# Kernel optimization log

Measured on AMD Instinct MI355X. Metric: run time of the kernel, lower is better.

The kernel has to match this reference:

```python
import jax, jax.numpy as jnp
import numpy as np

B, S, ENC_D, DEC_D, ATTN_D, OUT_D = 32, 2048, 1024, 1024, 1024, 1024
SCALING = 1.0


def setup_inputs() -> dict:
    key = jax.random.key(0)
    ks = jax.random.split(key, 10)
    enc_states = jax.random.normal(ks[0], (B, S, ENC_D), dtype=jnp.float32)
    # lengths in [S//2, S] so every row has at least one valid position
    enc_len = jax.random.randint(ks[1], (B,), S // 2, S + 1, dtype=jnp.int32)
    dec_states = jax.random.normal(ks[2], (B, DEC_D), dtype=jnp.float32)
    s = 0.02
    W_enc = jax.random.normal(ks[3], (ENC_D, ATTN_D), dtype=jnp.float32) * s
    b_enc = jnp.zeros((ATTN_D,), dtype=jnp.float32)
    W_dec = jax.random.normal(ks[4], (DEC_D, ATTN_D), dtype=jnp.float32) * s
    b_dec = jnp.zeros((ATTN_D,), dtype=jnp.float32)
    w_attn = jax.random.normal(ks[5], (ATTN_D,), dtype=jnp.float32) * s
    W_out = jax.random.normal(ks[6], (ENC_D, OUT_D), dtype=jnp.float32) * s
    b_out = jnp.zeros((OUT_D,), dtype=jnp.float32)
    return {
        "enc_states": enc_states,
        "dec_states": dec_states,
        "W_enc": W_enc, "b_enc": b_enc,
        "W_dec": W_dec, "b_dec": b_dec,
        "w_attn": w_attn,
        "W_out": W_out, "b_out": b_out,
        "enc_len": enc_len,
    }


def reference(enc_states, dec_states, W_enc, b_enc, W_dec, b_dec, w_attn, W_out, b_out, enc_len):
    # precomputed_enc_h = mlp_enc(enc_states): [B, S, ATTN_D]
    enc_h = jnp.einsum("bse,ea->bsa", enc_states, W_enc) + b_enc
    # dec_h = mlp_dec(dec_states): [B, ATTN_D]
    dec_h = dec_states @ W_dec + b_dec
    # additive (Bahdanau) score: tanh(enc_h + dec_h) . w_attn -> [B, S]
    attn = jnp.einsum("bsa,a->bs", jnp.tanh(enc_h + dec_h[:, None, :]), w_attn)
    # length mask
    mask = jnp.arange(enc_states.shape[1])[None, :] < enc_len[:, None]  # [B, S]
    attn = jnp.where(mask, attn, -jnp.inf)
    attn = jax.nn.softmax(attn * SCALING, axis=-1)
    # context = attn @ enc_states -> [B, ENC_D]
    context = jnp.einsum("bs,bse->be", attn, enc_states)
    context = context @ W_out + b_out
    return (context, attn)
```

## Files before the change

kernel.cpp:

```cpp
#include <hip/hip_runtime.h>
#include <cstdint>
#include <cstddef>

#define BATCH 32
#define SEQ   2048
#define DIM   1024
#define MROWS (BATCH*SEQ)

typedef __attribute__((ext_vector_type(4))) float  floatx4;
typedef __attribute__((ext_vector_type(8))) short  short8;

__device__ __forceinline__ unsigned short f2bf(float f) {
  unsigned int u = __float_as_uint(f);
  u += 0x7fffu + ((u >> 16) & 1u);
  return (unsigned short)(u >> 16);
}

__device__ __forceinline__ void async16(const void* g, void* l) {
  __builtin_amdgcn_global_load_lds(
      (const __attribute__((address_space(1))) unsigned int*)g,
      (__attribute__((address_space(3))) unsigned int*)l, 16, 0, 0);
}

__device__ __forceinline__ float fast_tanh(float x) {
  float e = __expf(2.0f * x);
  return 1.0f - 2.0f * __builtin_amdgcn_rcpf(1.0f + e);
}

__global__ void k_prep(const float* __restrict__ W_enc, unsigned short* __restrict__ Wt,
                       const float* __restrict__ dec, const float* __restrict__ W_dec,
                       const float* __restrict__ b_dec, const float* __restrict__ b_enc,
                       float* __restrict__ dech) {
  __shared__ float tile[32][33];
  int blk = blockIdx.x;
  int tid = threadIdx.x;
  if (blk < 1024) {
    int n0 = (blk & 31) * 32, k0 = (blk >> 5) * 32;
    int tx = tid & 31, ty = tid >> 5;
#pragma unroll
    for (int i = 0; i < 4; ++i) {
      int y = ty + i * 8;
      tile[y][tx] = W_enc[(size_t)(k0 + y) * DIM + n0 + tx];
    }
    __syncthreads();
#pragma unroll
    for (int i = 0; i < 4; ++i) {
      int y = ty + i * 8;
      Wt[(size_t)(n0 + y) * DIM + k0 + tx] = f2bf(tile[tx][y]);
    }
  } else {
    int db = blk - 1024;
    int ax = db & 3, bgi = (db >> 2) & 3, z = db >> 4;
    int a  = ax * 256 + tid;
    int bg = bgi * 8;
    float bias = (z == 0) ? (b_dec[a] + b_enc[a]) : 0.0f;
    float acc[8];
#pragma unroll
    for (int j = 0; j < 8; ++j) acc[j] = bias;
    const float* wcp = W_dec + (size_t)z * 128 * DIM + a;
#pragma unroll 4
    for (int e = 0; e < 128; ++e) {
      float w = wcp[(size_t)e * DIM];
#pragma unroll
      for (int j = 0; j < 8; ++j)
        acc[j] = fmaf(dec[(size_t)(bg + j) * DIM + z * 128 + e], w, acc[j]);
    }
#pragma unroll
    for (int j = 0; j < 8; ++j)
      atomicAdd(&dech[(size_t)(bg + j) * DIM + a], acc[j]);
  }
}

#define PH_BAR do { asm volatile("" ::: "memory"); __builtin_amdgcn_s_barrier(); asm volatile("" ::: "memory"); } while(0)
#define SCHED0 __builtin_amdgcn_sched_barrier(0)
#define SP1 __builtin_amdgcn_s_setprio(1)
#define SP0 __builtin_amdgcn_s_setprio(0)
#define VMCNT(n) asm volatile("s_waitcnt vmcnt(" #n ")" ::: "memory")
#define LGKM0 asm volatile("s_waitcnt lgkmcnt(0)" ::: "memory")

__global__ void __launch_bounds__(512, 2) k_gemm256(
    const float* __restrict__ enc,
    const unsigned short* __restrict__ Wt,
    const float* __restrict__ dech,
    const float* __restrict__ w_attn,
    const int* __restrict__ enc_len,
    float* __restrict__ score)
{
  int bid = blockIdx.x;
  int t  = (bid & 7) * 128 + (bid >> 3);
  int nb = t & 3;
  int rt = t >> 2;
  int bb = rt >> 3;
  int len = enc_len[bb];
  if (((rt & 7) * 256) >= len) return;

  __shared__ __align__(16) char lds[131072];

  int tid = threadIdx.x;
  int w = tid >> 6, lane = tid & 63;
  int wr = w >> 2;
  int wc = w & 3;
  int li = lane & 15, g = lane >> 4;
  int xl = (li & 7) << 4;

  const char* Agc = (const char*)enc + (size_t)rt * 256 * 4096;
  const char* Bg  = (const char*)(Wt + (size_t)nb * 256 * DIM);

  size_t sbase = (size_t)((lane >> 3) * 2048 +
                 (((lane & 7) << 4) ^ (((lane >> 3) & 7) << 4)));
  size_t swoff = (size_t)(w * 2) * 16384;
  int    ldbase = w * 2048;

#define STAGE_B(buf, h, kt) do { \
  async16(Bg + sbase + swoff + (size_t)(h) * 262144 + (size_t)(kt) * 128, \
          lds + 65536 + (buf) * 32768 + ldbase + (h) * 16384); \
  async16(Bg + sbase + swoff + 16384 + (size_t)(h) * 262144 + (size_t)(kt) * 128, \
          lds + 65536 + (buf) * 32768 + ldbase + 1024 + (h) * 16384); \
} while (0)

  size_t aoff = (size_t)(w * 16 + (lane >> 3)) * 4096 +
                (size_t)(((lane & 7) ^ (lane >> 3)) * 32);
  float4 aR[2][2][2];

#define LOAD_A(kt) do { \
  _Pragma("unroll") for (int c = 0; c < 2; ++c) { \
    const char* g0_ = Agc + aoff + (size_t)(c * 8) * 4096 + (size_t)(kt) * 256; \
    aR[0][c][0] = *(const float4*)(g0_); \
    aR[0][c][1] = *(const float4*)(g0_ + 16); \
  } \
} while (0)
#define LOAD_A1(kt) do { \
  _Pragma("unroll") for (int c = 0; c < 2; ++c) { \
    const char* g1_ = Agc + aoff + (size_t)(128 + c * 8) * 4096 + (size_t)(kt) * 256; \
    aR[1][c][0] = *(const float4*)(g1_); \
    aR[1][c][1] = *(const float4*)(g1_ + 16); \
  } \
} while (0)
#define WRITE_A(buf) do { \
  _Pragma("unroll") for (int h_ = 0; h_ < 2; ++h_) \
  _Pragma("unroll") for (int c_ = 0; c_ < 2; ++c_) { \
    float4 u0_ = aR[h_][c_][0], u1_ = aR[h_][c_][1]; \
    short8 pk_; \
    pk_[0] = (short)f2bf(u0_.x); pk_[1] = (short)f2bf(u0_.y); \
    pk_[2] = (short)f2bf(u0_.z); pk_[3] = (short)f2bf(u0_.w); \
    pk_[4] = (short)f2bf(u1_.x); pk_[5] = (short)f2bf(u1_.y); \
    pk_[6] = (short)f2bf(u1_.z); pk_[7] = (short)f2bf(u1_.w); \
    *(short8*)(lds + (buf) * 32768 + h_ * 16384 + w * 2048 + c_ * 1024 + lane * 16) = pk_; \
  } \
} while (0)

  short8 sA0[2][2], sA1[2][2];
  short8 aX[2][2];
  short8 bX[2][2];
  floatx4 acc[8][4] = {};

#define RD_A2(buf, f0, DST) do { \
  const char* base_ = lds + (buf) * 32768 + (wr * 128 + (f0) * 16 + li) * 128; \
  int c0_ = (g * 16) ^ xl; \
  _Pragma("unroll") for (int j = 0; j < 2; ++j) { \
    DST[j][0] = *(const short8*)(base_ + j * 2048 + c0_); \
    DST[j][1] = *(const short8*)(base_ + j * 2048 + (c0_ ^ 64)); \
  } \
} while (0)
#define RD_B(buf, nh, DST) do { \
  const char* base_ = lds + 65536 + (buf) * 32768 + (wc * 64 + (nh) * 32 + li) * 128; \
  int c0_ = (g * 16) ^ xl; \
  _Pragma("unroll") for (int tnq = 0; tnq < 2; ++tnq) { \
    DST[tnq][0] = *(const short8*)(base_ + tnq * 2048 + c0_); \
    DST[tnq][1] = *(const short8*)(base_ + tnq * 2048 + (c0_ ^ 64)); \
  } \
} while (0)
#define MFMA_Q(mh, nh, ALO, AHI, BB) do { \
  _Pragma("unroll") for (int ks = 0; ks < 2; ++ks) \
  _Pragma("unroll") for (int tnq = 0; tnq < 2; ++tnq) { \
    acc[(mh)*4+0][(nh)*2+tnq] = __builtin_amdgcn_mfma_f32_16x16x32_bf16(ALO[0][ks], BB[tnq][ks], acc[(mh)*4+0][(nh)*2+tnq], 0, 0, 0); \
    acc[(mh)*4+1][(nh)*2+tnq] = __builtin_amdgcn_mfma_f32_16x16x32_bf16(ALO[1][ks], BB[tnq][ks], acc[(mh)*4+1][(nh)*2+tnq], 0, 0, 0); \
    acc[(mh)*4+2][(nh)*2+tnq] = __builtin_amdgcn_mfma_f32_16x16x32_bf16(AHI[0][ks], BB[tnq][ks], acc[(mh)*4+2][(nh)*2+tnq], 0, 0, 0); \
    acc[(mh)*4+3][(nh)*2+tnq] = __builtin_amdgcn_mfma_f32_16x16x32_bf16(AHI[1][ks], BB[tnq][ks], acc[(mh)*4+3][(nh)*2+tnq], 0, 0, 0); \
  } \
} while (0)

#define TILE_STEP(CUR, KT2, MODE, SP_, SQ_) do { \
   \
  RD_A2(CUR, 2, aX); \
  RD_B(CUR, 0, bX); \
  if ((MODE) == 0) { LOAD_A(KT2); } \
  PH_BAR; SCHED0; SP1; MFMA_Q(0, 0, SP_, aX, bX); SP0; SCHED0; \
  PH_BAR; \
   \
  RD_B(CUR, 1, SQ_); \
  if ((MODE) == 0) { LOAD_A1(KT2); } \
  PH_BAR; SCHED0; SP1; MFMA_Q(0, 1, SP_, aX, SQ_); SP0; SCHED0; \
  PH_BAR; \
   \
  if ((MODE) == 0) { STAGE_B(CUR, 0, KT2); STAGE_B(CUR, 1, KT2); } \
  RD_A2(CUR, 4, SP_); \
  RD_A2(CUR, 6, aX); \
  PH_BAR; SCHED0; SP1; MFMA_Q(1, 1, SP_, aX, SQ_); SP0; SCHED0; \
  PH_BAR; \
   \
  if ((MODE) == 0) { VMCNT(4); WRITE_A(CUR); } \
  else if ((MODE) == 1) { VMCNT(0); } \
  if ((MODE) < 2) RD_A2((CUR) ^ 1, 0, SQ_); \
  PH_BAR; SCHED0; SP1; MFMA_Q(1, 0, SP_, aX, bX); SP0; SCHED0; \
  PH_BAR; \
} while (0)

  LOAD_A(0); LOAD_A1(0);
  VMCNT(0);
  WRITE_A(0);
  LOAD_A(1); LOAD_A1(1);
  STAGE_B(0, 0, 0); STAGE_B(0, 1, 0);
  STAGE_B(1, 0, 1); STAGE_B(1, 1, 1);
  VMCNT(4);
  WRITE_A(1);
  LGKM0;
  PH_BAR;
  RD_A2(0, 0, sA0);

#pragma unroll 1
  for (int u = 0; u < 14; u += 2) {
    TILE_STEP(0, u + 2, 0, sA0, sA1);
    TILE_STEP(1, u + 3, 0, sA1, sA0);
  }
  TILE_STEP(0, 0, 1, sA0, sA1);
  TILE_STEP(1, 0, 2, sA1, sA0);

  float dh[4], wa[4];
#pragma unroll
  for (int tn = 0; tn < 4; ++tn) {
    int n = nb * 256 + wc * 64 + tn * 16 + li;
    dh[tn] = dech[(size_t)bb * DIM + n];
    wa[tn] = w_attn[n];
  }
#pragma unroll
  for (int tm = 0; tm < 8; ++tm) {
    int mrow = rt * 256 + wr * 128 + tm * 16 + g * 4;
#pragma unroll
    for (int r = 0; r < 4; ++r) {
      float v = 0.0f;
#pragma unroll
      for (int tn = 0; tn < 4; ++tn)
        v = fmaf(wa[tn], fast_tanh(acc[tm][tn][r] + dh[tn]), v);
      v += __shfl_xor(v, 1);
      v += __shfl_xor(v, 2);
      v += __shfl_xor(v, 4);
      v += __shfl_xor(v, 8);
      if (li == 0) atomicAdd(&score[mrow + r], v);
    }
  }
#undef TILE_STEP
#undef MFMA_Q
#undef RD_B
#undef RD_A2
#undef WRITE_A
#undef LOAD_A1
#undef LOAD_A
#undef STAGE_B
}

__global__ void k_softmax(const float* __restrict__ score, const int* __restrict__ enc_len,
                          float* __restrict__ attn) {
  int b = blockIdx.x, tid = threadIdx.x;
  int len = enc_len[b];
  __shared__ float red[256];
  float v[8];
  float m = -1e30f;
#pragma unroll
  for (int i = 0; i < 8; ++i) {
    int s = tid + i * 256;
    v[i] = score[(size_t)b * SEQ + s];
    if (s < len) m = fmaxf(m, v[i]);
  }
  red[tid] = m; __syncthreads();
  for (int st = 128; st > 0; st >>= 1) {
    if (tid < st) red[tid] = fmaxf(red[tid], red[tid + st]);
    __syncthreads();
  }
  float mx = red[0]; __syncthreads();
  float sum = 0.0f;
#pragma unroll
  for (int i = 0; i < 8; ++i) {
    int s = tid + i * 256;
    float e = (s < len) ? __expf(v[i] - mx) : 0.0f;
    v[i] = e; sum += e;
  }
  red[tid] = sum; __syncthreads();
  for (int st = 128; st > 0; st >>= 1) {
    if (tid < st) red[tid] += red[tid + st];
    __syncthreads();
  }
  float inv = 1.0f / red[0];
#pragma unroll
  for (int i = 0; i < 8; ++i)
    attn[(size_t)b * SEQ + tid + i * 256] = v[i] * inv;
}

__global__ void k_context(const float* __restrict__ enc, const float* __restrict__ attn,
                          const int* __restrict__ enc_len, float* __restrict__ ctx) {
  int b = blockIdx.y, sc = blockIdx.x;
  int len = enc_len[b];
  int s0 = sc * 32;
  if (s0 >= len) return;
  int cnt = min(32, len - s0);
  int tid = threadIdx.x;
  const float* base = enc + ((size_t)b * SEQ + s0) * DIM + tid * 4;
  const float* ap   = attn + (size_t)b * SEQ + s0;
  float a0 = 0.f, a1 = 0.f, a2 = 0.f, a3 = 0.f;
  int i = 0;
  for (; i + 8 <= cnt; i += 8) {
    float4 x[8];
    float  w[8];
#pragma unroll
    for (int u = 0; u < 8; ++u)
      x[u] = *(const float4*)(base + (size_t)(i + u) * DIM);
#pragma unroll
    for (int u = 0; u < 8; ++u)
      w[u] = ap[i + u];
#pragma unroll
    for (int u = 0; u < 8; ++u) {
      a0 = fmaf(w[u], x[u].x, a0); a1 = fmaf(w[u], x[u].y, a1);
      a2 = fmaf(w[u], x[u].z, a2); a3 = fmaf(w[u], x[u].w, a3);
    }
  }
  for (; i < cnt; ++i) {
    float w = ap[i];
    float4 x = *(const float4*)(base + (size_t)i * DIM);
    a0 = fmaf(w, x.x, a0); a1 = fmaf(w, x.y, a1);
    a2 = fmaf(w, x.z, a2); a3 = fmaf(w, x.w, a3);
  }
  float* c = ctx + (size_t)b * DIM + tid * 4;
  atomicAdd(c + 0, a0); atomicAdd(c + 1, a1);
  atomicAdd(c + 2, a2); atomicAdd(c + 3, a3);
}

__global__ void k_out(const float* __restrict__ ctx, const float* __restrict__ W_out,
                      const float* __restrict__ b_out, float* __restrict__ out) {
  int o  = blockIdx.x * 256 + threadIdx.x;
  int bg = blockIdx.y * 8;
  int z  = blockIdx.z;
  float bias = (z == 0) ? b_out[o] : 0.0f;
  float acc[8];
#pragma unroll
  for (int j = 0; j < 8; ++j) acc[j] = bias;
  const float* wc = W_out + (size_t)z * 128 * DIM + o;
#pragma unroll 4
  for (int e = 0; e < 128; ++e) {
    float w = wc[(size_t)e * DIM];
#pragma unroll
    for (int j = 0; j < 8; ++j)
      acc[j] = fmaf(ctx[(size_t)(bg + j) * DIM + z * 128 + e], w, acc[j]);
  }
#pragma unroll
  for (int j = 0; j < 8; ++j)
    atomicAdd(&out[(size_t)(bg + j) * DIM + o], acc[j]);
}

extern "C" void kernel_launch(void* const* d_in, const int* in_sizes, int n_in,
                              void* d_out, int out_size, void* d_ws, size_t ws_size,
                              hipStream_t stream) {
  (void)in_sizes; (void)n_in; (void)out_size; (void)ws_size;
  const float* enc_states = (const float*)d_in[0];
  const float* dec_states = (const float*)d_in[1];
  const float* W_enc      = (const float*)d_in[2];
  const float* b_enc      = (const float*)d_in[3];
  const float* W_dec      = (const float*)d_in[4];
  const float* b_dec      = (const float*)d_in[5];
  const float* w_attn     = (const float*)d_in[6];
  const float* W_out      = (const float*)d_in[7];
  const float* b_out      = (const float*)d_in[8];
  const int*   enc_len    = (const int*)  d_in[9];

  float* out_ctx  = (float*)d_out;
  float* out_attn = (float*)d_out + BATCH * DIM;

  char* ws = (char*)d_ws;
  unsigned short* Wt  = (unsigned short*)ws;
  float* score = (float*)(ws + (2u << 20));
  float* ctx   = (float*)(ws + (2u << 20) + 262144);
  float* dech  = (float*)(ws + (2u << 20) + 262144 + 131072);

  hipMemsetAsync(ws + (2u << 20), 0, 262144 + 131072 + 131072, stream);
  hipMemsetAsync(d_out, 0, (size_t)BATCH * DIM * sizeof(float), stream);

  k_prep<<<1152, 256, 0, stream>>>(W_enc, Wt, dec_states, W_dec, b_dec, b_enc, dech);
  k_gemm256<<<1024, 512, 0, stream>>>(enc_states, Wt, dech, w_attn, enc_len, score);
  k_softmax<<<BATCH, 256, 0, stream>>>(score, enc_len, out_attn);
  k_context<<<dim3(64, BATCH), 256, 0, stream>>>(enc_states, out_attn, enc_len, ctx);
  k_out<<<dim3(4, 4, 8), 256, 0, stream>>>(ctx, W_out, b_out, out_ctx);
}
```

Measured before the change: 671.8 us.

## Pre-convert encoder states to bf16 and make each GEMM block sweep all N tiles

Encoder states are now converted to bf16 once in the prep kernel, for valid rows only, and written to a workspace buffer. The GEMM loads A tiles asynchronously into LDS instead of converting them per block. The GEMM grid shrinks from 1024 to 256 blocks, and each block loops over all four 256-column N tiles with an epilogue after each. This removes the fourfold re-reading and re-conversion of fp32 activations, at the cost of an extra write and read pass over a bf16 copy. Only 256 blocks at 2 per CU may underfill the GPU, and the masked-out tail blocks now leave whole CUs idle.

```diff
diff --git a/kernel.cpp b/kernel.cpp
--- a/kernel.cpp
+++ b/kernel.cpp
@@ -27,7 +27,9 @@
   return 1.0f - 2.0f * __builtin_amdgcn_rcpf(1.0f + e);
 }
 
-__global__ void k_prep(const float* __restrict__ W_enc, unsigned short* __restrict__ Wt,
+__global__ void k_prep(const float* __restrict__ enc, const int* __restrict__ enc_len,
+                       unsigned short* __restrict__ Abf,
+                       const float* __restrict__ W_enc, unsigned short* __restrict__ Wt,
                        const float* __restrict__ dec, const float* __restrict__ W_dec,
                        const float* __restrict__ b_dec, const float* __restrict__ b_enc,
                        float* __restrict__ dech) {
@@ -48,7 +50,7 @@
       int y = ty + i * 8;
       Wt[(size_t)(n0 + y) * DIM + k0 + tx] = f2bf(tile[tx][y]);
     }
-  } else {
+  } else if (blk < 1152) {
     int db = blk - 1024;
     int ax = db & 3, bgi = (db >> 2) & 3, z = db >> 4;
     int a  = ax * 256 + tid;
@@ -68,6 +70,21 @@
 #pragma unroll
     for (int j = 0; j < 8; ++j)
       atomicAdd(&dech[(size_t)(bg + j) * DIM + a], acc[j]);
+  } else {
+    int cv = blk - 1152;
+    int b = cv >> 8, rc = cv & 255;
+    int r0 = rc * 8;
+    if (r0 >= enc_len[b]) return;
+    size_t base = ((size_t)b * SEQ + r0) * DIM;
+    const float4* src = (const float4*)(enc + base);
+    ushort4* dst = (ushort4*)(Abf + base);
+#pragma unroll
+    for (int i = 0; i < 8; ++i) {
+      float4 v = src[tid + i * 256];
+      ushort4 h;
+      h.x = f2bf(v.x); h.y = f2bf(v.y); h.z = f2bf(v.z); h.w = f2bf(v.w);
+      dst[tid + i * 256] = h;
+    }
   }
 }
 
@@ -76,20 +93,16 @@
 #define SP1 __builtin_amdgcn_s_setprio(1)
 #define SP0 __builtin_amdgcn_s_setprio(0)
 #define VMCNT(n) asm volatile("s_waitcnt vmcnt(" #n ")" ::: "memory")
-#define LGKM0 asm volatile("s_waitcnt lgkmcnt(0)" ::: "memory")
 
 __global__ void __launch_bounds__(512, 2) k_gemm256(
-    const float* __restrict__ enc,
+    const unsigned short* __restrict__ Abf,
     const unsigned short* __restrict__ Wt,
     const float* __restrict__ dech,
     const float* __restrict__ w_attn,
     const int* __restrict__ enc_len,
     float* __restrict__ score)
 {
-  int bid = blockIdx.x;
-  int t  = (bid & 7) * 128 + (bid >> 3);
-  int nb = t & 3;
-  int rt = t >> 2;
+  int rt = blockIdx.x;
   int bb = rt >> 3;
   int len = enc_len[bb];
   if (((rt & 7) * 256) >= len) return;
@@ -103,50 +116,27 @@
   int li = lane & 15, g = lane >> 4;
   int xl = (li & 7) << 4;
 
-  const char* Agc = (const char*)enc + (size_t)rt * 256 * 4096;
-  const char* Bg  = (const char*)(Wt + (size_t)nb * 256 * DIM);
+  const char* Ag = (const char*)(Abf + (size_t)rt * 256 * DIM);
+  const char* Bg = (const char*)Wt;
 
   size_t sbase = (size_t)((lane >> 3) * 2048 +
                  (((lane & 7) << 4) ^ (((lane >> 3) & 7) << 4)));
   size_t swoff = (size_t)(w * 2) * 16384;
   int    ldbase = w * 2048;
 
-#define STAGE_B(buf, h, kt) do { \
-  async16(Bg + sbase + swoff + (size_t)(h) * 262144 + (size_t)(kt) * 128, \
+#define STAGE_A(buf, h, V) do { \
+  size_t ka_ = (size_t)((V) & 15) * 128; \
+  async16(Ag + sbase + swoff + (size_t)(h) * 262144 + ka_, \
+          lds + (buf) * 32768 + ldbase + (h) * 16384); \
+  async16(Ag + sbase + swoff + 16384 + (size_t)(h) * 262144 + ka_, \
+          lds + (buf) * 32768 + ldbase + 1024 + (h) * 16384); \
+} while (0)
+#define STAGE_B(buf, h, V) do { \
+  size_t kb_ = (size_t)((V) >> 4) * 524288 + (size_t)((V) & 15) * 128; \
+  async16(Bg + kb_ + sbase + swoff + (size_t)(h) * 262144, \
           lds + 65536 + (buf) * 32768 + ldbase + (h) * 16384); \
-  async16(Bg + sbase + swoff + 16384 + (size_t)(h) * 262144 + (size_t)(kt) * 128, \
+  async16(Bg + kb_ + sbase + swoff + 16384 + (size_t)(h) * 262144, \
           lds + 65536 + (buf) * 32768 + ldbase + 1024 + (h) * 16384); \
-} while (0)
-
-  size_t aoff = (size_t)(w * 16 + (lane >> 3)) * 4096 +
-                (size_t)(((lane & 7) ^ (lane >> 3)) * 32);
-  float4 aR[2][2][2];
-
-#define LOAD_A(kt) do { \
-  _Pragma("unroll") for (int c = 0; c < 2; ++c) { \
-    const char* g0_ = Agc + aoff + (size_t)(c * 8) * 4096 + (size_t)(kt) * 256; \
-    aR[0][c][0] = *(const float4*)(g0_); \
-    aR[0][c][1] = *(const float4*)(g0_ + 16); \
-  } \
-} while (0)
-#define LOAD_A1(kt) do { \
-  _Pragma("unroll") for (int c = 0; c < 2; ++c) { \
-    const char* g1_ = Agc + aoff + (size_t)(128 + c * 8) * 4096 + (size_t)(kt) * 256; \
-    aR[1][c][0] = *(const float4*)(g1_); \
-    aR[1][c][1] = *(const float4*)(g1_ + 16); \
-  } \
-} while (0)
-#define WRITE_A(buf) do { \
-  _Pragma("unroll") for (int h_ = 0; h_ < 2; ++h_) \
-  _Pragma("unroll") for (int c_ = 0; c_ < 2; ++c_) { \
-    float4 u0_ = aR[h_][c_][0], u1_ = aR[h_][c_][1]; \
-    short8 pk_; \
-    pk_[0] = (short)f2bf(u0_.x); pk_[1] = (short)f2bf(u0_.y); \
-    pk_[2] = (short)f2bf(u0_.z); pk_[3] = (short)f2bf(u0_.w); \
-    pk_[4] = (short)f2bf(u1_.x); pk_[5] = (short)f2bf(u1_.y); \
-    pk_[6] = (short)f2bf(u1_.z); pk_[7] = (short)f2bf(u1_.w); \
-    *(short8*)(lds + (buf) * 32768 + h_ * 16384 + w * 2048 + c_ * 1024 + lane * 16) = pk_; \
-  } \
 } while (0)
 
   short8 sA0[2][2], sA1[2][2];
@@ -180,83 +170,77 @@
   } \
 } while (0)
 
-#define TILE_STEP(CUR, KT2, MODE, SP_, SQ_) do { \
-   \
+#define TILE_STEP(CUR, V2, MODE, SP_, SQ_) do { \
   RD_A2(CUR, 2, aX); \
   RD_B(CUR, 0, bX); \
-  if ((MODE) == 0) { LOAD_A(KT2); } \
   PH_BAR; SCHED0; SP1; MFMA_Q(0, 0, SP_, aX, bX); SP0; SCHED0; \
   PH_BAR; \
-   \
   RD_B(CUR, 1, SQ_); \
-  if ((MODE) == 0) { LOAD_A1(KT2); } \
   PH_BAR; SCHED0; SP1; MFMA_Q(0, 1, SP_, aX, SQ_); SP0; SCHED0; \
   PH_BAR; \
-   \
-  if ((MODE) == 0) { STAGE_B(CUR, 0, KT2); STAGE_B(CUR, 1, KT2); } \
+  if ((MODE) == 0) { STAGE_B(CUR, 0, V2); STAGE_B(CUR, 1, V2); } \
   RD_A2(CUR, 4, SP_); \
   RD_A2(CUR, 6, aX); \
   PH_BAR; SCHED0; SP1; MFMA_Q(1, 1, SP_, aX, SQ_); SP0; SCHED0; \
   PH_BAR; \
-   \
-  if ((MODE) == 0) { VMCNT(4); WRITE_A(CUR); } \
-  else if ((MODE) == 1) { VMCNT(0); } \
+  if ((MODE) == 0) { STAGE_A(CUR, 0, V2); STAGE_A(CUR, 1, V2); } \
+  if ((MODE) == 0) { VMCNT(8); } else if ((MODE) == 1) { VMCNT(0); } \
   if ((MODE) < 2) RD_A2((CUR) ^ 1, 0, SQ_); \
   PH_BAR; SCHED0; SP1; MFMA_Q(1, 0, SP_, aX, bX); SP0; SCHED0; \
   PH_BAR; \
 } while (0)
 
-  LOAD_A(0); LOAD_A1(0);
-  VMCNT(0);
-  WRITE_A(0);
-  LOAD_A(1); LOAD_A1(1);
-  STAGE_B(0, 0, 0); STAGE_B(0, 1, 0);
-  STAGE_B(1, 0, 1); STAGE_B(1, 1, 1);
-  VMCNT(4);
-  WRITE_A(1);
-  LGKM0;
+#define EPI(NB) do { \
+  float dh_[4], wa_[4]; \
+  _Pragma("unroll") for (int tn = 0; tn < 4; ++tn) { \
+    int n_ = (NB) * 256 + wc * 64 + tn * 16 + li; \
+    dh_[tn] = dech[(size_t)bb * DIM + n_]; \
+    wa_[tn] = w_attn[n_]; \
+  } \
+  _Pragma("unroll") for (int tm = 0; tm < 8; ++tm) { \
+    int mrow_ = rt * 256 + wr * 128 + tm * 16 + g * 4; \
+    _Pragma("unroll") for (int r = 0; r < 4; ++r) { \
+      float v_ = 0.0f; \
+      _Pragma("unroll") for (int tn = 0; tn < 4; ++tn) \
+        v_ = fmaf(wa_[tn], fast_tanh(acc[tm][tn][r] + dh_[tn]), v_); \
+      v_ += __shfl_xor(v_, 1); \
+      v_ += __shfl_xor(v_, 2); \
+      v_ += __shfl_xor(v_, 4); \
+      v_ += __shfl_xor(v_, 8); \
+      if (li == 0) atomicAdd(&score[mrow_ + r], v_); \
+    } \
+  } \
+  _Pragma("unroll") for (int tm = 0; tm < 8; ++tm) \
+  _Pragma("unroll") for (int tn = 0; tn < 4; ++tn) \
+  _Pragma("unroll") for (int r = 0; r < 4; ++r) \
+    acc[tm][tn][r] = 0.0f; \
+} while (0)
+
+  STAGE_B(0, 0, 0); STAGE_B(0, 1, 0); STAGE_A(0, 0, 0); STAGE_A(0, 1, 0);
+  STAGE_B(1, 0, 1); STAGE_B(1, 1, 1); STAGE_A(1, 0, 1); STAGE_A(1, 1, 1);
+  VMCNT(8);
   PH_BAR;
   RD_A2(0, 0, sA0);
 
 #pragma unroll 1
-  for (int u = 0; u < 14; u += 2) {
-    TILE_STEP(0, u + 2, 0, sA0, sA1);
-    TILE_STEP(1, u + 3, 0, sA1, sA0);
+  for (int v = 0; v < 62; v += 2) {
+    TILE_STEP(0, v + 2, 0, sA0, sA1);
+    TILE_STEP(1, v + 3, 0, sA1, sA0);
+    if ((v & 15) == 14) {
+      EPI(v >> 4);
+    }
   }
   TILE_STEP(0, 0, 1, sA0, sA1);
   TILE_STEP(1, 0, 2, sA1, sA0);
-
-  float dh[4], wa[4];
-#pragma unroll
-  for (int tn = 0; tn < 4; ++tn) {
-    int n = nb * 256 + wc * 64 + tn * 16 + li;
-    dh[tn] = dech[(size_t)bb * DIM + n];
-    wa[tn] = w_attn[n];
-  }
-#pragma unroll
-  for (int tm = 0; tm < 8; ++tm) {
-    int mrow = rt * 256 + wr * 128 + tm * 16 + g * 4;
-#pragma unroll
-    for (int r = 0; r < 4; ++r) {
-      float v = 0.0f;
-#pragma unroll
-      for (int tn = 0; tn < 4; ++tn)
-        v = fmaf(wa[tn], fast_tanh(acc[tm][tn][r] + dh[tn]), v);
-      v += __shfl_xor(v, 1);
-      v += __shfl_xor(v, 2);
-      v += __shfl_xor(v, 4);
-      v += __shfl_xor(v, 8);
-      if (li == 0) atomicAdd(&score[mrow + r], v);
-    }
-  }
+  EPI(3);
+
+#undef EPI
 #undef TILE_STEP
 #undef MFMA_Q
 #undef RD_B
 #undef RD_A2
-#undef WRITE_A
-#undef LOAD_A1
-#undef LOAD_A
 #undef STAGE_B
+#undef STAGE_A
 }
 
 __global__ void k_softmax(const float* __restrict__ score, const int* __restrict__ enc_len,
@@ -379,12 +363,14 @@
   float* score = (float*)(ws + (2u << 20));
   float* ctx   = (float*)(ws + (2u << 20) + 262144);
   float* dech  = (float*)(ws + (2u << 20) + 262144 + 131072);
+  unsigned short* Abf = (unsigned short*)(ws + (3u << 20));
 
   hipMemsetAsync(ws + (2u << 20), 0, 262144 + 131072 + 131072, stream);
   hipMemsetAsync(d_out, 0, (size_t)BATCH * DIM * sizeof(float), stream);
 
-  k_prep<<<1152, 256, 0, stream>>>(W_enc, Wt, dec_states, W_dec, b_dec, b_enc, dech);
-  k_gemm256<<<1024, 512, 0, stream>>>(enc_states, Wt, dech, w_attn, enc_len, score);
+  k_prep<<<9344, 256, 0, stream>>>(enc_states, enc_len, Abf,
+                                   W_enc, Wt, dec_states, W_dec, b_dec, b_enc, dech);
+  k_gemm256<<<256, 512, 0, stream>>>(Abf, Wt, dech, w_attn, enc_len, score);
   k_softmax<<<BATCH, 256, 0, stream>>>(score, enc_len, out_attn);
   k_context<<<dim3(64, BATCH), 256, 0, stream>>>(enc_states, out_attn, enc_len, ctx);
   k_out<<<dim3(4, 4, 8), 256, 0, stream>>>(ctx, W_out, b_out, out_ctx);
```

Result: faster. 579.7 us (-13.7%).
